# Kernel optimization log

Hardware: AMD Instinct MI355X
Metric: run time of the kernel (lower is better)

The kernel has to match this reference:

```python
import jax, jax.numpy as jnp
import numpy as np

SIGMA = 1.0


def _rbf_kernel(X, sigma):
    # pairwise squared Euclidean distances: ||xi||^2 + ||xj||^2 - 2 xi.xj
    sq = jnp.sum(X * X, axis=1)  # [n]
    d2 = sq[:, None] + sq[None, :] - 2.0 * (X @ X.T)
    d2 = jnp.maximum(d2, 0.0)
    return jnp.exp(-d2 / (2.0 * sigma ** 2))


def _center(K):
    # Kc = H @ K @ H with H = I - 11^T/n, done in O(n^2):
    # Kc = K - row_mean - col_mean + grand_mean
    row_mean = jnp.mean(K, axis=1, keepdims=True)   # [n,1]
    col_mean = jnp.mean(K, axis=0, keepdims=True)   # [1,n]
    grand = jnp.mean(K)
    return K - row_mean - col_mean + grand


def setup_inputs() -> dict:
    key = jax.random.key(0)
    k1, k2 = jax.random.split(key)
    X = jax.random.normal(k1, (8192, 512), dtype=jnp.float32)
    Y = jax.random.normal(k2, (8192, 512), dtype=jnp.float32)
    return {"X": X, "Y": Y}


def reference(X, Y):
    n = X.shape[0]
    K = _rbf_kernel(X, SIGMA)
    L = _rbf_kernel(Y, SIGMA)
    Kc = _center(K)
    Lc = _center(L)
    # trace(Kc @ Lc) == sum(Kc * Lc^T) == sum(Kc * Lc) since Lc symmetric
    hsic_value = jnp.sum(Kc * Lc) / (n - 1) ** 2
    return hsic_value
```

## Files before the change

kernel.cpp:

```cpp
#include <hip/hip_runtime.h>
#include <hip/hip_bf16.h>

#define N 8192
#define D 512

typedef __attribute__((ext_vector_type(4))) float f32x4;
typedef __attribute__((ext_vector_type(2))) long i64x2;

#define WAITVM(n) asm volatile("s_waitcnt vmcnt(" #n ")" ::: "memory")
#define BAR __builtin_amdgcn_s_barrier()

__device__ __forceinline__ void g2l16(const void* g, void* l) {
  __builtin_amdgcn_global_load_lds(
      (const __attribute__((address_space(1))) void*)g,
      (__attribute__((address_space(3))) void*)l, 16, 0, 0);
}

__global__ __launch_bounds__(128) void prep_kernel(
    const float* __restrict__ X, const float* __restrict__ Y,
    unsigned char* __restrict__ Xb, unsigned char* __restrict__ Yb,
    float* __restrict__ sqX, float* __restrict__ sqY) {
  const int b = blockIdx.x;
  const int row = b & (N - 1);
  const float* src = (b < N) ? X : Y;
  unsigned char* dst = (b < N) ? Xb : Yb;
  float* sq = (b < N) ? sqX : sqY;
  const int t = threadIdx.x;
  float4 v = reinterpret_cast<const float4*>(src + (size_t)row * D)[t];
  unsigned p = __builtin_amdgcn_cvt_pk_fp8_f32(v.x, v.y, 0, false);
  p = __builtin_amdgcn_cvt_pk_fp8_f32(v.z, v.w, p, true);
  float f0 = __builtin_amdgcn_cvt_f32_fp8(p, 0);
  float f1 = __builtin_amdgcn_cvt_f32_fp8(p, 1);
  float f2 = __builtin_amdgcn_cvt_f32_fp8(p, 2);
  float f3 = __builtin_amdgcn_cvt_f32_fp8(p, 3);
  float s = f0 * f0 + f1 * f1 + f2 * f2 + f3 * f3;
  const int g = t >> 4;
  const int kl = (t & 15) * 4;
  const int dest = g * 64 + ((kl & 31) >> 3) * 16 + (kl >> 5) * 8 + (kl & 7);
  *reinterpret_cast<unsigned*>(dst + (size_t)row * D + dest) = p;
  #pragma unroll
  for (int msk = 1; msk < 64; msk <<= 1) s += __shfl_xor(s, msk);
  __shared__ float red[2];
  if ((t & 63) == 0) red[t >> 6] = s;
  __syncthreads();
  if (t == 0) sq[row] = red[0] + red[1];
}

__global__ __launch_bounds__(256, 2) void hsic_main(
    const unsigned char* __restrict__ Xb, const unsigned char* __restrict__ Yb,
    const float* __restrict__ sqX, const float* __restrict__ sqY,
    float* __restrict__ rowK, float* __restrict__ rowL,
    float* __restrict__ sums) {
  __shared__ __align__(16) unsigned char sbuf[2][2][128 * 128];

  const int bid = (blockIdx.x & 7) * 260 + (blockIdx.x >> 3);
  int ti = (int)((129.0f - sqrtf(16641.0f - 8.0f * (float)bid)) * 0.5f);
  while (ti > 0 && (ti * (129 - ti)) / 2 > bid) --ti;
  while (((ti + 1) * (128 - ti)) / 2 <= bid) ++ti;
  const int tj = ti + (bid - (ti * (129 - ti)) / 2);
  const bool diag = (ti == tj);

  const int ib = ti * 128, jb = tj * 128;
  const int t = threadIdx.x;
  const int lane = t & 63, wave = t >> 6;
  const int wr = wave >> 1, wc = wave & 1;
  const int fr = lane & 15, fq = lane >> 4;

  f32x4 accK[4][4], accL[4][4];
  #pragma unroll
  for (int m = 0; m < 4; ++m)
    #pragma unroll
    for (int n = 0; n < 4; ++n) { accK[m][n] = (f32x4)0.f; accL[m][n] = (f32x4)0.f; }

  const unsigned char* s0 = Xb + (size_t)ib * D;
  const unsigned char* s1 = Xb + (size_t)jb * D;
  const unsigned char* s2 = Yb + (size_t)ib * D;
  const unsigned char* s3 = Yb + (size_t)jb * D;

  const int srow = t >> 3;
  const int swcb = ((t & 7) * 16) ^ (((t >> 3) & 7) << 4);
  const int lo16 = t * 16;

  auto stage = [&](int ph) {
    const int kt = ph >> 1;
    const unsigned char* si = (ph & 1) ? s2 : s0;
    const unsigned char* sj = (ph & 1) ? s3 : s1;
    unsigned char* di = sbuf[ph & 1][0];
    unsigned char* dj = sbuf[ph & 1][1];
    #pragma unroll
    for (int q = 0; q < 4; ++q) {
      const size_t goff = (size_t)(q * 32 + srow) * D + kt * 128 + swcb;
      const int lo = q * 4096 + lo16;
      g2l16(si + goff, di + lo);
      g2l16(sj + goff, dj + lo);
    }
  };

  auto compute = [&](const unsigned char* si, const unsigned char* sj,
                     f32x4 (&acc)[4][4]) {
    #pragma unroll
    for (int kk = 0; kk < 2; ++kk) {
      const int csel = kk * 64 + fq * 16;
      i64x2 a[4], b[4];
      #pragma unroll
      for (int m = 0; m < 4; ++m) {
        const int row = wr * 64 + m * 16 + fr;
        a[m] = *(const i64x2*)&si[row * 128 + (csel ^ ((fr & 7) << 4))];
      }
      #pragma unroll
      for (int n = 0; n < 4; ++n) {
        const int row = wc * 64 + n * 16 + fr;
        b[n] = *(const i64x2*)&sj[row * 128 + (csel ^ ((fr & 7) << 4))];
      }
      __builtin_amdgcn_s_setprio(1);
      #pragma unroll
      for (int m = 0; m < 4; ++m)
        #pragma unroll
        for (int n = 0; n < 4; ++n) {
          acc[m][n] = __builtin_amdgcn_mfma_f32_16x16x32_fp8_fp8(a[m][0], b[n][0], acc[m][n], 0, 0, 0);
          acc[m][n] = __builtin_amdgcn_mfma_f32_16x16x32_fp8_fp8(a[m][1], b[n][1], acc[m][n], 0, 0, 0);
        }
      __builtin_amdgcn_s_setprio(0);
    }
  };

  stage(0); stage(1);
  #pragma unroll 1
  for (int kt = 0; kt < 3; ++kt) {
    WAITVM(8);
    BAR;
    compute(sbuf[0][0], sbuf[0][1], accK);
    BAR;
    stage(2 * kt + 2);
    WAITVM(8);
    BAR;
    compute(sbuf[1][0], sbuf[1][1], accL);
    BAR;
    stage(2 * kt + 3);
  }
  WAITVM(8);
  BAR;
  compute(sbuf[0][0], sbuf[0][1], accK);
  WAITVM(0);
  BAR;
  compute(sbuf[1][0], sbuf[1][1], accL);

  float sxj[4], syj[4];
  #pragma unroll
  for (int n = 0; n < 4; ++n) {
    const int j = jb + wc * 64 + n * 16 + fr;
    sxj[n] = sqX[j];
    syj[n] = sqY[j];
  }
  float kl = 0.f;
  float ckK[4] = {0.f, 0.f, 0.f, 0.f}, ckL[4] = {0.f, 0.f, 0.f, 0.f};
  #pragma unroll
  for (int m = 0; m < 4; ++m) {
    #pragma unroll
    for (int r = 0; r < 4; ++r) {
      const int i = ib + wr * 64 + m * 16 + fq * 4 + r;
      const float sxi = sqX[i], syi = sqY[i];
      float rk = 0.f, rl = 0.f;
      #pragma unroll
      for (int n = 0; n < 4; ++n) {
        float dK = fmaxf(sxi + sxj[n] - 2.f * accK[m][n][r], 0.f);
        float Kv = __expf(-0.5f * dK);
        float dL = fmaxf(syi + syj[n] - 2.f * accL[m][n][r], 0.f);
        float Lv = __expf(-0.5f * dL);
        kl += Kv * Lv;
        rk += Kv; rl += Lv;
        ckK[n] += Kv; ckL[n] += Lv;
      }
      #pragma unroll
      for (int msk = 1; msk < 16; msk <<= 1) {
        rk += __shfl_xor(rk, msk);
        rl += __shfl_xor(rl, msk);
      }
      if (fr == 0) {
        atomicAdd(&rowK[i], rk);
        atomicAdd(&rowL[i], rl);
      }
    }
  }
  if (!diag) {
    #pragma unroll
    for (int n = 0; n < 4; ++n) {
      float a2 = ckK[n], b2 = ckL[n];
      a2 += __shfl_xor(a2, 16); a2 += __shfl_xor(a2, 32);
      b2 += __shfl_xor(b2, 16); b2 += __shfl_xor(b2, 32);
      if (fq == 0) {
        const int j = jb + wc * 64 + n * 16 + fr;
        atomicAdd(&rowK[j], a2);
        atomicAdd(&rowL[j], b2);
      }
    }
    kl *= 2.f;
  }
  #pragma unroll
  for (int msk = 1; msk < 64; msk <<= 1) kl += __shfl_xor(kl, msk);
  __shared__ float klred[4];
  if (lane == 0) klred[wave] = kl;
  __syncthreads();
  if (t == 0) atomicAdd(sums, klred[0] + klred[1] + klred[2] + klred[3]);
}

__global__ __launch_bounds__(256) void finalize_kernel(
    const float* __restrict__ rowK, const float* __restrict__ rowL,
    const float* __restrict__ sums, float* __restrict__ out) {
  const int t = threadIdx.x;
  float dp = 0.f, sk = 0.f, sl = 0.f;
  for (int i = t; i < N; i += 256) {
    float a = rowK[i], b = rowL[i];
    dp += a * b; sk += a; sl += b;
  }
  #pragma unroll
  for (int msk = 1; msk < 64; msk <<= 1) {
    dp += __shfl_xor(dp, msk);
    sk += __shfl_xor(sk, msk);
    sl += __shfl_xor(sl, msk);
  }
  __shared__ float r[3][4];
  const int wave = t >> 6, lane = t & 63;
  if (lane == 0) { r[0][wave] = dp; r[1][wave] = sk; r[2][wave] = sl; }
  __syncthreads();
  if (t == 0) {
    float DP = r[0][0] + r[0][1] + r[0][2] + r[0][3];
    float SK = r[1][0] + r[1][1] + r[1][2] + r[1][3];
    float SL = r[2][0] + r[2][1] + r[2][2] + r[2][3];
    const float n = (float)N;
    float raw = sums[0] - (2.f / n) * DP + (SK / n) * (SL / n);
    out[0] = raw / ((n - 1.f) * (n - 1.f));
  }
}

extern "C" void kernel_launch(void* const* d_in, const int* in_sizes, int n_in,
                              void* d_out, int out_size, void* d_ws, size_t ws_size,
                              hipStream_t stream) {
  const float* X = (const float*)d_in[0];
  const float* Y = (const float*)d_in[1];
  char* ws = (char*)d_ws;
  unsigned char* Xb = (unsigned char*)ws;
  unsigned char* Yb = (unsigned char*)(ws + (size_t)N * D);
  float* sqX = (float*)(ws + (size_t)2 * N * D);
  float* sqY = sqX + N;
  float* rowK = sqY + N;
  float* rowL = rowK + N;
  float* sums = rowL + N;

  hipMemsetAsync(rowK, 0, (size_t)(2 * N + 16) * sizeof(float), stream);
  prep_kernel<<<2 * N, 128, 0, stream>>>(X, Y, Xb, Yb, sqX, sqY);
  const int ntiles = (N / 128) * (N / 128 + 1) / 2;
  hsic_main<<<ntiles, 256, 0, stream>>>(Xb, Yb, sqX, sqY, rowK, rowL, sums);
  finalize_kernel<<<1, 256, 0, stream>>>(rowK, rowL, sums, (float*)d_out);
}
```

Baseline: 150.6 us.

## Compute K then L sequentially with one accumulator set to raise occupancy

The main kernel now computes the X Gram tile fully, converts the K values to packed fp8 in registers, and only then computes the Y Gram tile, reusing a single accumulator array instead of two. The LDS staging buffer is halved by using a K-step of 64 bytes, with a new swizzle. Launch bounds go from 2 to 4 blocks per SM. The aim is to cut register and LDS pressure so more waves can hide memory latency. In exchange K is stored in fp8 for the K·L product, which lowers accuracy, and the pipeline now has more, shorter iterations with extra barriers.

```diff
diff --git a/kernel.cpp b/kernel.cpp
--- a/kernel.cpp
+++ b/kernel.cpp
@@ -8,6 +8,7 @@
 typedef __attribute__((ext_vector_type(2))) long i64x2;
 
 #define WAITVM(n) asm volatile("s_waitcnt vmcnt(" #n ")" ::: "memory")
+#define WAITLGKM asm volatile("s_waitcnt lgkmcnt(0)" ::: "memory")
 #define BAR __builtin_amdgcn_s_barrier()
 
 __device__ __forceinline__ void g2l16(const void* g, void* l) {
@@ -46,12 +47,12 @@
   if (t == 0) sq[row] = red[0] + red[1];
 }
 
-__global__ __launch_bounds__(256, 2) void hsic_main(
+__global__ __launch_bounds__(256, 4) void hsic_main(
     const unsigned char* __restrict__ Xb, const unsigned char* __restrict__ Yb,
     const float* __restrict__ sqX, const float* __restrict__ sqY,
     float* __restrict__ rowK, float* __restrict__ rowL,
     float* __restrict__ sums) {
-  __shared__ __align__(16) unsigned char sbuf[2][2][128 * 128];
+  __shared__ __align__(16) unsigned char sbuf[2][2][128 * 64];
 
   const int bid = (blockIdx.x & 7) * 260 + (blockIdx.x >> 3);
   int ti = (int)((129.0f - sqrtf(16641.0f - 8.0f * (float)bid)) * 0.5f);
@@ -66,133 +67,164 @@
   const int wr = wave >> 1, wc = wave & 1;
   const int fr = lane & 15, fq = lane >> 4;
 
-  f32x4 accK[4][4], accL[4][4];
+  f32x4 acc[4][4];
   #pragma unroll
   for (int m = 0; m < 4; ++m)
     #pragma unroll
-    for (int n = 0; n < 4; ++n) { accK[m][n] = (f32x4)0.f; accL[m][n] = (f32x4)0.f; }
+    for (int n = 0; n < 4; ++n) acc[m][n] = (f32x4)0.f;
 
   const unsigned char* s0 = Xb + (size_t)ib * D;
   const unsigned char* s1 = Xb + (size_t)jb * D;
   const unsigned char* s2 = Yb + (size_t)ib * D;
   const unsigned char* s3 = Yb + (size_t)jb * D;
 
-  const int srow = t >> 3;
-  const int swcb = ((t & 7) * 16) ^ (((t >> 3) & 7) << 4);
+  const int srow = t >> 2;
+  const int swcb = ((t & 3) * 16) ^ (((t >> 3) & 3) << 4);
   const int lo16 = t * 16;
 
-  auto stage = [&](int ph) {
-    const int kt = ph >> 1;
-    const unsigned char* si = (ph & 1) ? s2 : s0;
-    const unsigned char* sj = (ph & 1) ? s3 : s1;
-    unsigned char* di = sbuf[ph & 1][0];
-    unsigned char* dj = sbuf[ph & 1][1];
-    #pragma unroll
-    for (int q = 0; q < 4; ++q) {
-      const size_t goff = (size_t)(q * 32 + srow) * D + kt * 128 + swcb;
+  auto stage = [&](int kt, int p, bool isY) {
+    const unsigned char* si = isY ? s2 : s0;
+    const unsigned char* sj = isY ? s3 : s1;
+    #pragma unroll
+    for (int q = 0; q < 2; ++q) {
+      const size_t goff = (size_t)(q * 64 + srow) * D + kt * 64 + swcb;
       const int lo = q * 4096 + lo16;
-      g2l16(si + goff, di + lo);
-      g2l16(sj + goff, dj + lo);
+      g2l16(si + goff, &sbuf[p][0][lo]);
+      g2l16(sj + goff, &sbuf[p][1][lo]);
     }
   };
 
-  auto compute = [&](const unsigned char* si, const unsigned char* sj,
-                     f32x4 (&acc)[4][4]) {
-    #pragma unroll
-    for (int kk = 0; kk < 2; ++kk) {
-      const int csel = kk * 64 + fq * 16;
-      i64x2 a[4], b[4];
-      #pragma unroll
-      for (int m = 0; m < 4; ++m) {
-        const int row = wr * 64 + m * 16 + fr;
-        a[m] = *(const i64x2*)&si[row * 128 + (csel ^ ((fr & 7) << 4))];
-      }
+  const int fcol = (fq * 16) ^ (((fr >> 1) & 3) << 4);
+
+  i64x2 a[4], b[4];
+  auto frags = [&](int p) {
+    const unsigned char* si = sbuf[p][0];
+    const unsigned char* sj = sbuf[p][1];
+    #pragma unroll
+    for (int m = 0; m < 4; ++m)
+      a[m] = *(const i64x2*)&si[(wr * 64 + m * 16 + fr) * 64 + fcol];
+    #pragma unroll
+    for (int n = 0; n < 4; ++n)
+      b[n] = *(const i64x2*)&sj[(wc * 64 + n * 16 + fr) * 64 + fcol];
+  };
+  auto mma = [&]() {
+    __builtin_amdgcn_s_setprio(1);
+    #pragma unroll
+    for (int m = 0; m < 4; ++m)
       #pragma unroll
       for (int n = 0; n < 4; ++n) {
-        const int row = wc * 64 + n * 16 + fr;
-        b[n] = *(const i64x2*)&sj[row * 128 + (csel ^ ((fr & 7) << 4))];
-      }
-      __builtin_amdgcn_s_setprio(1);
-      #pragma unroll
-      for (int m = 0; m < 4; ++m)
+        acc[m][n] = __builtin_amdgcn_mfma_f32_16x16x32_fp8_fp8(a[m][0], b[n][0], acc[m][n], 0, 0, 0);
+        acc[m][n] = __builtin_amdgcn_mfma_f32_16x16x32_fp8_fp8(a[m][1], b[n][1], acc[m][n], 0, 0, 0);
+      }
+    __builtin_amdgcn_s_setprio(0);
+  };
+
+  stage(0, 0, false); stage(1, 1, false);
+  #pragma unroll 1
+  for (int kt = 0; kt < 6; ++kt) {
+    WAITVM(4); BAR;
+    frags(kt & 1);
+    WAITLGKM; BAR;
+    stage(kt + 2, kt & 1, false);
+    mma();
+  }
+  WAITVM(4); BAR; frags(0); WAITLGKM; BAR;
+  stage(0, 0, true);
+  mma();
+  WAITVM(4); BAR; frags(1); WAITLGKM; BAR;
+  stage(1, 1, true);
+  mma();
+
+  unsigned kp[16];
+  {
+    float sxj[4];
+    #pragma unroll
+    for (int n = 0; n < 4; ++n) sxj[n] = sqX[jb + wc * 64 + n * 16 + fr];
+    float ckK[4] = {0.f, 0.f, 0.f, 0.f};
+    #pragma unroll
+    for (int m = 0; m < 4; ++m) {
+      #pragma unroll
+      for (int r = 0; r < 4; ++r) {
+        const int i = ib + wr * 64 + m * 16 + fq * 4 + r;
+        const float sxi = sqX[i];
+        float Kv[4];
+        float rk = 0.f;
         #pragma unroll
         for (int n = 0; n < 4; ++n) {
-          acc[m][n] = __builtin_amdgcn_mfma_f32_16x16x32_fp8_fp8(a[m][0], b[n][0], acc[m][n], 0, 0, 0);
-          acc[m][n] = __builtin_amdgcn_mfma_f32_16x16x32_fp8_fp8(a[m][1], b[n][1], acc[m][n], 0, 0, 0);
+          float dK = fmaxf(sxi + sxj[n] - 2.f * acc[m][n][r], 0.f);
+          Kv[n] = __expf(-0.5f * dK);
+          rk += Kv[n];
+          ckK[n] += Kv[n];
         }
-      __builtin_amdgcn_s_setprio(0);
-    }
-  };
-
-  stage(0); stage(1);
+        unsigned pk = __builtin_amdgcn_cvt_pk_fp8_f32(Kv[0], Kv[1], 0, false);
+        kp[m * 4 + r] = __builtin_amdgcn_cvt_pk_fp8_f32(Kv[2], Kv[3], pk, true);
+        #pragma unroll
+        for (int msk = 1; msk < 16; msk <<= 1) rk += __shfl_xor(rk, msk);
+        if (fr == 0) atomicAdd(&rowK[i], rk);
+      }
+    }
+    if (!diag) {
+      #pragma unroll
+      for (int n = 0; n < 4; ++n) {
+        float a2 = ckK[n];
+        a2 += __shfl_xor(a2, 16); a2 += __shfl_xor(a2, 32);
+        if (fq == 0) atomicAdd(&rowK[jb + wc * 64 + n * 16 + fr], a2);
+      }
+    }
+  }
+
+  #pragma unroll
+  for (int m = 0; m < 4; ++m)
+    #pragma unroll
+    for (int n = 0; n < 4; ++n) acc[m][n] = (f32x4)0.f;
+
   #pragma unroll 1
-  for (int kt = 0; kt < 3; ++kt) {
-    WAITVM(8);
-    BAR;
-    compute(sbuf[0][0], sbuf[0][1], accK);
-    BAR;
-    stage(2 * kt + 2);
-    WAITVM(8);
-    BAR;
-    compute(sbuf[1][0], sbuf[1][1], accL);
-    BAR;
-    stage(2 * kt + 3);
-  }
-  WAITVM(8);
-  BAR;
-  compute(sbuf[0][0], sbuf[0][1], accK);
-  WAITVM(0);
-  BAR;
-  compute(sbuf[1][0], sbuf[1][1], accL);
-
-  float sxj[4], syj[4];
-  #pragma unroll
-  for (int n = 0; n < 4; ++n) {
-    const int j = jb + wc * 64 + n * 16 + fr;
-    sxj[n] = sqX[j];
-    syj[n] = sqY[j];
-  }
+  for (int kt = 0; kt < 6; ++kt) {
+    WAITVM(4); BAR;
+    frags(kt & 1);
+    WAITLGKM; BAR;
+    stage(kt + 2, kt & 1, true);
+    mma();
+  }
+  WAITVM(4); BAR; frags(0); WAITLGKM; mma();
+  WAITVM(0); BAR; frags(1); WAITLGKM; mma();
+
+  float sxj[4];
+  #pragma unroll
+  for (int n = 0; n < 4; ++n) sxj[n] = sqY[jb + wc * 64 + n * 16 + fr];
   float kl = 0.f;
-  float ckK[4] = {0.f, 0.f, 0.f, 0.f}, ckL[4] = {0.f, 0.f, 0.f, 0.f};
+  float ckL[4] = {0.f, 0.f, 0.f, 0.f};
   #pragma unroll
   for (int m = 0; m < 4; ++m) {
     #pragma unroll
     for (int r = 0; r < 4; ++r) {
       const int i = ib + wr * 64 + m * 16 + fq * 4 + r;
-      const float sxi = sqX[i], syi = sqY[i];
-      float rk = 0.f, rl = 0.f;
+      const float syi = sqY[i];
+      const unsigned pk = kp[m * 4 + r];
+      const float Kvv[4] = {__builtin_amdgcn_cvt_f32_fp8(pk, 0),
+                            __builtin_amdgcn_cvt_f32_fp8(pk, 1),
+                            __builtin_amdgcn_cvt_f32_fp8(pk, 2),
+                            __builtin_amdgcn_cvt_f32_fp8(pk, 3)};
+      float rl = 0.f;
       #pragma unroll
       for (int n = 0; n < 4; ++n) {
-        float dK = fmaxf(sxi + sxj[n] - 2.f * accK[m][n][r], 0.f);
-        float Kv = __expf(-0.5f * dK);
-        float dL = fmaxf(syi + syj[n] - 2.f * accL[m][n][r], 0.f);
+        float dL = fmaxf(syi + sxj[n] - 2.f * acc[m][n][r], 0.f);
         float Lv = __expf(-0.5f * dL);
-        kl += Kv * Lv;
-        rk += Kv; rl += Lv;
-        ckK[n] += Kv; ckL[n] += Lv;
-      }
-      #pragma unroll
-      for (int msk = 1; msk < 16; msk <<= 1) {
-        rk += __shfl_xor(rk, msk);
-        rl += __shfl_xor(rl, msk);
-      }
-      if (fr == 0) {
-        atomicAdd(&rowK[i], rk);
-        atomicAdd(&rowL[i], rl);
-      }
+        kl += Kvv[n] * Lv;
+        rl += Lv;
+        ckL[n] += Lv;
+      }
+      #pragma unroll
+      for (int msk = 1; msk < 16; msk <<= 1) rl += __shfl_xor(rl, msk);
+      if (fr == 0) atomicAdd(&rowL[i], rl);
     }
   }
   if (!diag) {
     #pragma unroll
     for (int n = 0; n < 4; ++n) {
-      float a2 = ckK[n], b2 = ckL[n];
-      a2 += __shfl_xor(a2, 16); a2 += __shfl_xor(a2, 32);
+      float b2 = ckL[n];
       b2 += __shfl_xor(b2, 16); b2 += __shfl_xor(b2, 32);
-      if (fq == 0) {
-        const int j = jb + wc * 64 + n * 16 + fr;
-        atomicAdd(&rowK[j], a2);
-        atomicAdd(&rowL[j], b2);
-      }
+      if (fq == 0) atomicAdd(&rowL[jb + wc * 64 + n * 16 + fr], b2);
     }
     kl *= 2.f;
   }
@@ -247,7 +279,7 @@
   float* rowL = rowK + N;
   float* sums = rowL + N;
 
-  hipMemsetAsync(rowK, 0, (size_t)(2 * N + 16) * sizeof(float), stream);
+  (void)hipMemsetAsync(rowK, 0, (size_t)(2 * N + 16) * sizeof(float), stream);
   prep_kernel<<<2 * N, 128, 0, stream>>>(X, Y, Xb, Yb, sqX, sqY);
   const int ntiles = (N / 128) * (N / 128 + 1) / 2;
   hsic_main<<<ntiles, 256, 0, stream>>>(Xb, Yb, sqX, sqY, rowK, rowL, sums);
```

After: 174.8 us. 1.16x slower.

## Triple-buffer 64-byte K slices with one barrier per phase in HSIC GEMM

Applied to the files above, without the earlier changes.

The main loop changes from two 128-byte-deep LDS buffers, each with two barriers per phase, to three 64-byte-deep buffers cycled across 16 phases. Each phase has one barrier, reads its fragments into registers, issues the global-to-LDS prefetch two phases ahead, then runs the MFMAs for K or L. The aim is to cut barrier stalls and hide load latency better. LDS use also drops from 64KB to 48KB, which could help occupancy. The cost is twice as many pipeline steps, each with less work, and a new swizzle that matches the 64-byte row width.

```diff
diff --git a/kernel.cpp b/kernel.cpp
--- a/kernel.cpp
+++ b/kernel.cpp
@@ -51,7 +51,7 @@
     const float* __restrict__ sqX, const float* __restrict__ sqY,
     float* __restrict__ rowK, float* __restrict__ rowL,
     float* __restrict__ sums) {
-  __shared__ __align__(16) unsigned char sbuf[2][2][128 * 128];
+  __shared__ __align__(16) unsigned char sbuf[3][2][128 * 64];
 
   const int bid = (blockIdx.x & 7) * 260 + (blockIdx.x >> 3);
   int ti = (int)((129.0f - sqrtf(16641.0f - 8.0f * (float)bid)) * 0.5f);
@@ -77,73 +77,77 @@
   const unsigned char* s2 = Yb + (size_t)ib * D;
   const unsigned char* s3 = Yb + (size_t)jb * D;
 
-  const int srow = t >> 3;
-  const int swcb = ((t & 7) * 16) ^ (((t >> 3) & 7) << 4);
+  const int srow = t >> 2;
+  const int swcb = ((t & 3) * 16) ^ (((t >> 3) & 3) << 4);
   const int lo16 = t * 16;
 
   auto stage = [&](int ph) {
+    const int b = ph % 3;
     const int kt = ph >> 1;
     const unsigned char* si = (ph & 1) ? s2 : s0;
     const unsigned char* sj = (ph & 1) ? s3 : s1;
-    unsigned char* di = sbuf[ph & 1][0];
-    unsigned char* dj = sbuf[ph & 1][1];
-    #pragma unroll
-    for (int q = 0; q < 4; ++q) {
-      const size_t goff = (size_t)(q * 32 + srow) * D + kt * 128 + swcb;
+    #pragma unroll
+    for (int q = 0; q < 2; ++q) {
+      const size_t goff = (size_t)(q * 64 + srow) * D + kt * 64 + swcb;
       const int lo = q * 4096 + lo16;
-      g2l16(si + goff, di + lo);
-      g2l16(sj + goff, dj + lo);
+      g2l16(si + goff, &sbuf[b][0][lo]);
+      g2l16(sj + goff, &sbuf[b][1][lo]);
     }
   };
 
-  auto compute = [&](const unsigned char* si, const unsigned char* sj,
-                     f32x4 (&acc)[4][4]) {
-    #pragma unroll
-    for (int kk = 0; kk < 2; ++kk) {
-      const int csel = kk * 64 + fq * 16;
-      i64x2 a[4], b[4];
-      #pragma unroll
-      for (int m = 0; m < 4; ++m) {
-        const int row = wr * 64 + m * 16 + fr;
-        a[m] = *(const i64x2*)&si[row * 128 + (csel ^ ((fr & 7) << 4))];
-      }
+  const int fcol = (fq * 16) ^ (((fr >> 1) & 3) << 4);
+
+  i64x2 a[4], b[4];
+  auto frags = [&](int ph) {
+    const unsigned char* si = sbuf[ph % 3][0];
+    const unsigned char* sj = sbuf[ph % 3][1];
+    #pragma unroll
+    for (int m = 0; m < 4; ++m)
+      a[m] = *(const i64x2*)&si[(wr * 64 + m * 16 + fr) * 64 + fcol];
+    #pragma unroll
+    for (int n = 0; n < 4; ++n)
+      b[n] = *(const i64x2*)&sj[(wc * 64 + n * 16 + fr) * 64 + fcol];
+  };
+  auto mmaK = [&]() {
+    __builtin_amdgcn_s_setprio(1);
+    #pragma unroll
+    for (int m = 0; m < 4; ++m)
       #pragma unroll
       for (int n = 0; n < 4; ++n) {
-        const int row = wc * 64 + n * 16 + fr;
-        b[n] = *(const i64x2*)&sj[row * 128 + (csel ^ ((fr & 7) << 4))];
-      }
-      __builtin_amdgcn_s_setprio(1);
-      #pragma unroll
-      for (int m = 0; m < 4; ++m)
-        #pragma unroll
-        for (int n = 0; n < 4; ++n) {
-          acc[m][n] = __builtin_amdgcn_mfma_f32_16x16x32_fp8_fp8(a[m][0], b[n][0], acc[m][n], 0, 0, 0);
-          acc[m][n] = __builtin_amdgcn_mfma_f32_16x16x32_fp8_fp8(a[m][1], b[n][1], acc[m][n], 0, 0, 0);
-        }
-      __builtin_amdgcn_s_setprio(0);
-    }
+        accK[m][n] = __builtin_amdgcn_mfma_f32_16x16x32_fp8_fp8(a[m][0], b[n][0], accK[m][n], 0, 0, 0);
+        accK[m][n] = __builtin_amdgcn_mfma_f32_16x16x32_fp8_fp8(a[m][1], b[n][1], accK[m][n], 0, 0, 0);
+      }
+    __builtin_amdgcn_s_setprio(0);
+  };
+  auto mmaL = [&]() {
+    __builtin_amdgcn_s_setprio(1);
+    #pragma unroll
+    for (int m = 0; m < 4; ++m)
+      #pragma unroll
+      for (int n = 0; n < 4; ++n) {
+        accL[m][n] = __builtin_amdgcn_mfma_f32_16x16x32_fp8_fp8(a[m][0], b[n][0], accL[m][n], 0, 0, 0);
+        accL[m][n] = __builtin_amdgcn_mfma_f32_16x16x32_fp8_fp8(a[m][1], b[n][1], accL[m][n], 0, 0, 0);
+      }
+    __builtin_amdgcn_s_setprio(0);
   };
 
   stage(0); stage(1);
   #pragma unroll 1
-  for (int kt = 0; kt < 3; ++kt) {
-    WAITVM(8);
+  for (int p = 0; p < 14; ++p) {
+    WAITVM(4);
     BAR;
-    compute(sbuf[0][0], sbuf[0][1], accK);
-    BAR;
-    stage(2 * kt + 2);
-    WAITVM(8);
-    BAR;
-    compute(sbuf[1][0], sbuf[1][1], accL);
-    BAR;
-    stage(2 * kt + 3);
-  }
-  WAITVM(8);
+    frags(p);
+    stage(p + 2);
+    if (p & 1) mmaL(); else mmaK();
+  }
+  WAITVM(4);
   BAR;
-  compute(sbuf[0][0], sbuf[0][1], accK);
+  frags(14);
+  mmaK();
   WAITVM(0);
   BAR;
-  compute(sbuf[1][0], sbuf[1][1], accL);
+  frags(15);
+  mmaL();
 
   float sxj[4], syj[4];
   #pragma unroll
@@ -247,7 +251,7 @@
   float* rowL = rowK + N;
   float* sums = rowL + N;
 
-  hipMemsetAsync(rowK, 0, (size_t)(2 * N + 16) * sizeof(float), stream);
+  (void)hipMemsetAsync(rowK, 0, (size_t)(2 * N + 16) * sizeof(float), stream);
   prep_kernel<<<2 * N, 128, 0, stream>>>(X, Y, Xb, Yb, sqX, sqY);
   const int ntiles = (N / 128) * (N / 128 + 1) / 2;
   hsic_main<<<ntiles, 256, 0, stream>>>(Xb, Yb, sqX, sqY, rowK, rowL, sums);
```

Result: slower. 164.7 us (+9.3%).

## Switch to single-wave 64x64 tiles with barrier-free fused K/L staging

Applied to the files above, without the earlier changes.

Replaces the 4-wave 128x128 tile kernel with a one-wave-per-block 64x64 tile kernel over 8256 triangular tiles. Each k-step loads the X and Y slices together into one set of 4KB LDS buffers. The next stage is issued right after the LDS reads drain, so no workgroup barriers are needed, and K and L MFMAs are interleaved. The intent is to remove barrier stalls and to hide latency through much higher occupancy. The cost is halved operand reuse, which doubles global and LDS traffic, and twice as many row-sum atomics.

```diff
diff --git a/kernel.cpp b/kernel.cpp
--- a/kernel.cpp
+++ b/kernel.cpp
@@ -8,7 +8,7 @@
 typedef __attribute__((ext_vector_type(2))) long i64x2;
 
 #define WAITVM(n) asm volatile("s_waitcnt vmcnt(" #n ")" ::: "memory")
-#define BAR __builtin_amdgcn_s_barrier()
+#define WAITLGKM asm volatile("s_waitcnt lgkmcnt(0)" ::: "memory")
 
 __device__ __forceinline__ void g2l16(const void* g, void* l) {
   __builtin_amdgcn_global_load_lds(
@@ -46,25 +46,26 @@
   if (t == 0) sq[row] = red[0] + red[1];
 }
 
-__global__ __launch_bounds__(256, 2) void hsic_main(
+__global__ __launch_bounds__(64) void hsic_main(
     const unsigned char* __restrict__ Xb, const unsigned char* __restrict__ Yb,
     const float* __restrict__ sqX, const float* __restrict__ sqY,
     float* __restrict__ rowK, float* __restrict__ rowL,
     float* __restrict__ sums) {
-  __shared__ __align__(16) unsigned char sbuf[2][2][128 * 128];
-
-  const int bid = (blockIdx.x & 7) * 260 + (blockIdx.x >> 3);
-  int ti = (int)((129.0f - sqrtf(16641.0f - 8.0f * (float)bid)) * 0.5f);
-  while (ti > 0 && (ti * (129 - ti)) / 2 > bid) --ti;
-  while (((ti + 1) * (128 - ti)) / 2 <= bid) ++ti;
-  const int tj = ti + (bid - (ti * (129 - ti)) / 2);
+  __shared__ __align__(16) unsigned char sXi[4096];
+  __shared__ __align__(16) unsigned char sXj[4096];
+  __shared__ __align__(16) unsigned char sYi[4096];
+  __shared__ __align__(16) unsigned char sYj[4096];
+
+  const int bid = (blockIdx.x & 7) * 1032 + (blockIdx.x >> 3);
+  int ti = (int)((257.0f - sqrtf(66049.0f - 8.0f * (float)bid)) * 0.5f);
+  while (ti > 0 && (ti * (257 - ti)) / 2 > bid) --ti;
+  while (((ti + 1) * (256 - ti)) / 2 <= bid) ++ti;
+  const int tj = ti + (bid - (ti * (257 - ti)) / 2);
   const bool diag = (ti == tj);
 
-  const int ib = ti * 128, jb = tj * 128;
+  const int ib = ti * 64, jb = tj * 64;
   const int t = threadIdx.x;
-  const int lane = t & 63, wave = t >> 6;
-  const int wr = wave >> 1, wc = wave & 1;
-  const int fr = lane & 15, fq = lane >> 4;
+  const int fr = t & 15, fq = t >> 4;
 
   f32x4 accK[4][4], accL[4][4];
   #pragma unroll
@@ -77,78 +78,60 @@
   const unsigned char* s2 = Yb + (size_t)ib * D;
   const unsigned char* s3 = Yb + (size_t)jb * D;
 
-  const int srow = t >> 3;
-  const int swcb = ((t & 7) * 16) ^ (((t >> 3) & 7) << 4);
+  const int srow = t >> 2;
+  const int swcb = ((t & 3) * 16) ^ (((t >> 3) & 3) << 4);
   const int lo16 = t * 16;
 
-  auto stage = [&](int ph) {
-    const int kt = ph >> 1;
-    const unsigned char* si = (ph & 1) ? s2 : s0;
-    const unsigned char* sj = (ph & 1) ? s3 : s1;
-    unsigned char* di = sbuf[ph & 1][0];
-    unsigned char* dj = sbuf[ph & 1][1];
+  auto stage = [&](int kt) {
     #pragma unroll
     for (int q = 0; q < 4; ++q) {
-      const size_t goff = (size_t)(q * 32 + srow) * D + kt * 128 + swcb;
-      const int lo = q * 4096 + lo16;
-      g2l16(si + goff, di + lo);
-      g2l16(sj + goff, dj + lo);
+      const size_t goff = (size_t)(q * 16 + srow) * D + kt * 64 + swcb;
+      const int lo = q * 1024 + lo16;
+      g2l16(s0 + goff, sXi + lo);
+      g2l16(s1 + goff, sXj + lo);
+      g2l16(s2 + goff, sYi + lo);
+      g2l16(s3 + goff, sYj + lo);
     }
   };
 
-  auto compute = [&](const unsigned char* si, const unsigned char* sj,
-                     f32x4 (&acc)[4][4]) {
-    #pragma unroll
-    for (int kk = 0; kk < 2; ++kk) {
-      const int csel = kk * 64 + fq * 16;
-      i64x2 a[4], b[4];
-      #pragma unroll
-      for (int m = 0; m < 4; ++m) {
-        const int row = wr * 64 + m * 16 + fr;
-        a[m] = *(const i64x2*)&si[row * 128 + (csel ^ ((fr & 7) << 4))];
-      }
+  const int fcol = (fq * 16) ^ (((fr >> 1) & 3) << 4);
+
+  #pragma unroll 1
+  for (int kt = 0; kt < 8; ++kt) {
+    if (kt == 0) stage(0);
+    WAITVM(0);
+    i64x2 ax[4], bx[4], ay[4], by[4];
+    #pragma unroll
+    for (int m = 0; m < 4; ++m) {
+      const int ro = (m * 16 + fr) * 64 + fcol;
+      ax[m] = *(const i64x2*)&sXi[ro];
+      ay[m] = *(const i64x2*)&sYi[ro];
+    }
+    #pragma unroll
+    for (int n = 0; n < 4; ++n) {
+      const int ro = (n * 16 + fr) * 64 + fcol;
+      bx[n] = *(const i64x2*)&sXj[ro];
+      by[n] = *(const i64x2*)&sYj[ro];
+    }
+    WAITLGKM;
+    if (kt < 7) stage(kt + 1);
+    __builtin_amdgcn_s_setprio(1);
+    #pragma unroll
+    for (int m = 0; m < 4; ++m)
       #pragma unroll
       for (int n = 0; n < 4; ++n) {
-        const int row = wc * 64 + n * 16 + fr;
-        b[n] = *(const i64x2*)&sj[row * 128 + (csel ^ ((fr & 7) << 4))];
-      }
-      __builtin_amdgcn_s_setprio(1);
-      #pragma unroll
-      for (int m = 0; m < 4; ++m)
-        #pragma unroll
-        for (int n = 0; n < 4; ++n) {
-          acc[m][n] = __builtin_amdgcn_mfma_f32_16x16x32_fp8_fp8(a[m][0], b[n][0], acc[m][n], 0, 0, 0);
-          acc[m][n] = __builtin_amdgcn_mfma_f32_16x16x32_fp8_fp8(a[m][1], b[n][1], acc[m][n], 0, 0, 0);
-        }
-      __builtin_amdgcn_s_setprio(0);
-    }
-  };
-
-  stage(0); stage(1);
-  #pragma unroll 1
-  for (int kt = 0; kt < 3; ++kt) {
-    WAITVM(8);
-    BAR;
-    compute(sbuf[0][0], sbuf[0][1], accK);
-    BAR;
-    stage(2 * kt + 2);
-    WAITVM(8);
-    BAR;
-    compute(sbuf[1][0], sbuf[1][1], accL);
-    BAR;
-    stage(2 * kt + 3);
-  }
-  WAITVM(8);
-  BAR;
-  compute(sbuf[0][0], sbuf[0][1], accK);
-  WAITVM(0);
-  BAR;
-  compute(sbuf[1][0], sbuf[1][1], accL);
+        accK[m][n] = __builtin_amdgcn_mfma_f32_16x16x32_fp8_fp8(ax[m][0], bx[n][0], accK[m][n], 0, 0, 0);
+        accK[m][n] = __builtin_amdgcn_mfma_f32_16x16x32_fp8_fp8(ax[m][1], bx[n][1], accK[m][n], 0, 0, 0);
+        accL[m][n] = __builtin_amdgcn_mfma_f32_16x16x32_fp8_fp8(ay[m][0], by[n][0], accL[m][n], 0, 0, 0);
+        accL[m][n] = __builtin_amdgcn_mfma_f32_16x16x32_fp8_fp8(ay[m][1], by[n][1], accL[m][n], 0, 0, 0);
+      }
+    __builtin_amdgcn_s_setprio(0);
+  }
 
   float sxj[4], syj[4];
   #pragma unroll
   for (int n = 0; n < 4; ++n) {
-    const int j = jb + wc * 64 + n * 16 + fr;
+    const int j = jb + n * 16 + fr;
     sxj[n] = sqX[j];
     syj[n] = sqY[j];
   }
@@ -158,7 +141,7 @@
   for (int m = 0; m < 4; ++m) {
     #pragma unroll
     for (int r = 0; r < 4; ++r) {
-      const int i = ib + wr * 64 + m * 16 + fq * 4 + r;
+      const int i = ib + m * 16 + fq * 4 + r;
       const float sxi = sqX[i], syi = sqY[i];
       float rk = 0.f, rl = 0.f;
       #pragma unroll
@@ -189,7 +172,7 @@
       a2 += __shfl_xor(a2, 16); a2 += __shfl_xor(a2, 32);
       b2 += __shfl_xor(b2, 16); b2 += __shfl_xor(b2, 32);
       if (fq == 0) {
-        const int j = jb + wc * 64 + n * 16 + fr;
+        const int j = jb + n * 16 + fr;
         atomicAdd(&rowK[j], a2);
         atomicAdd(&rowL[j], b2);
       }
@@ -198,10 +181,7 @@
   }
   #pragma unroll
   for (int msk = 1; msk < 64; msk <<= 1) kl += __shfl_xor(kl, msk);
-  __shared__ float klred[4];
-  if (lane == 0) klred[wave] = kl;
-  __syncthreads();
-  if (t == 0) atomicAdd(sums, klred[0] + klred[1] + klred[2] + klred[3]);
+  if (t == 0) atomicAdd(sums, kl);
 }
 
 __global__ __launch_bounds__(256) void finalize_kernel(
@@ -247,9 +227,9 @@
   float* rowL = rowK + N;
   float* sums = rowL + N;
 
-  hipMemsetAsync(rowK, 0, (size_t)(2 * N + 16) * sizeof(float), stream);
+  (void)hipMemsetAsync(rowK, 0, (size_t)(2 * N + 16) * sizeof(float), stream);
   prep_kernel<<<2 * N, 128, 0, stream>>>(X, Y, Xb, Yb, sqX, sqY);
-  const int ntiles = (N / 128) * (N / 128 + 1) / 2;
-  hsic_main<<<ntiles, 256, 0, stream>>>(Xb, Yb, sqX, sqY, rowK, rowL, sums);
+  const int ntiles = 128 * 129 / 2;
+  hsic_main<<<ntiles, 64, 0, stream>>>(Xb, Yb, sqX, sqY, rowK, rowL, sums);
   finalize_kernel<<<1, 256, 0, stream>>>(rowK, rowL, sums, (float*)d_out);
 }
```

Measured after the change: 219.5 us. +45.7%, slower.
